# Optimization experiments

Hardware: AMD Instinct MI355X
Metric: run time of the kernel (lower is better)

Reference implementation:

```python
import jax, jax.numpy as jnp
import numpy as np

N, E = 50000, 800000
IN, HID, OUT = 128, 128, 64
BN_EPS = 1e-5


def _w(key, fan_in, fan_out):
    return jax.random.normal(key, (fan_in, fan_out), dtype=jnp.float32) / np.sqrt(fan_in)


def setup_inputs() -> dict:
    key = jax.random.key(0)
    ks = jax.random.split(key, 12)
    x = jax.random.normal(ks[0], (N, IN), dtype=jnp.float32)
    src = jax.random.randint(ks[1], (E,), 0, N, dtype=jnp.int32)
    dst = jax.random.randint(ks[2], (E,), 0, N, dtype=jnp.int32)
    eps = jax.random.normal(ks[3], (N, OUT), dtype=jnp.float32)
    return {
        "x": x, "src": src, "dst": dst, "eps": eps,
        # SAGEConv 1: in -> hidden (lin_l has bias, lin_r no bias, mean aggr)
        "W1l": _w(ks[4], IN, HID), "W1r": _w(ks[5], IN, HID), "b1": jnp.zeros((HID,), jnp.float32),
        "g1": jnp.ones((HID,), jnp.float32), "be1": jnp.zeros((HID,), jnp.float32),
        # SAGEConv 2: hidden -> 2*hidden
        "W2l": _w(ks[6], HID, 2 * HID), "W2r": _w(ks[7], HID, 2 * HID), "b2": jnp.zeros((2 * HID,), jnp.float32),
        "g2": jnp.ones((2 * HID,), jnp.float32), "be2": jnp.zeros((2 * HID,), jnp.float32),
        # SAGEConv 3: 2*hidden -> 2*out
        "W3l": _w(ks[8], 2 * HID, 2 * OUT), "W3r": _w(ks[9], 2 * HID, 2 * OUT), "b3": jnp.zeros((2 * OUT,), jnp.float32),
    }


def _sage(h, src, dst, Wl, Wr, b):
    # mean-aggregate source features at destination nodes, then two GEMMs
    msg = jax.ops.segment_sum(h[src], dst, num_segments=N)          # [N, F]
    deg = jax.ops.segment_sum(jnp.ones((src.shape[0],), h.dtype), dst, num_segments=N)
    aggr = msg / jnp.maximum(deg, 1.0)[:, None]
    return aggr @ Wl + h @ Wr + b


def _bn(h, gamma, beta):
    m = jnp.mean(h, axis=0)
    v = jnp.var(h, axis=0)
    return gamma * (h - m) * jax.lax.rsqrt(v + BN_EPS) + beta


def reference(x, src, dst, eps, W1l, W1r, b1, g1, be1, W2l, W2r, b2, g2, be2, W3l, W3r, b3):
    h = jax.nn.relu(_sage(x, src, dst, W1l, W1r, b1))
    h = _bn(h, g1, be1)                       # dropout = identity (eval)
    h = jax.nn.relu(_sage(h, src, dst, W2l, W2r, b2))
    h = _bn(h, g2, be2)
    h = _sage(h, src, dst, W3l, W3r, b3)      # [N, 2*OUT]
    mean, log_std = jnp.split(h, 2, axis=-1)
    z = mean + jnp.exp(log_std) * eps         # reparameterize
    return z
```

## Files before the change

### kernel.cpp

```cpp
#include <hip/hip_runtime.h>
#include <math.h>

#define N_NODES 50000
#define N_EDGES 800000
#define BN_EPS_F 1e-5f
#define SCAN_BS 512
#define SCAN_NB 98
#define RC 391
#define RQ 49
#define GXP 392

typedef unsigned short ushort_t;
typedef unsigned int uint_t;
typedef __attribute__((ext_vector_type(8))) short bf16x8;
typedef __attribute__((ext_vector_type(4))) float f32x4;

static __device__ __forceinline__ float4 ld4(const float* p) {
    return *reinterpret_cast<const float4*>(p);
}
static __device__ __forceinline__ float bf2f(ushort_t u) {
    return __uint_as_float(((uint_t)u) << 16);
}
static __device__ __forceinline__ ushort_t f2b(float f) {
    uint_t u = __float_as_uint(f);
    u += 0x7fffu + ((u >> 16) & 1u);
    return (ushort_t)(u >> 16);
}
static __device__ __forceinline__ void gload16(const void* g, void* l) {
    __builtin_amdgcn_global_load_lds(
        (const __attribute__((address_space(1))) void*)g,
        (__attribute__((address_space(3))) void*)l, 16, 0, 0);
}


__global__ void k_zero_i32(int* __restrict__ p, int n) {
    int i = blockIdx.x * blockDim.x + threadIdx.x;
    if (i < n) p[i] = 0;
}

__global__ void k_pre(const int* __restrict__ dst, int* __restrict__ deg2,
                      ushort_t* __restrict__ rank,
                      const float* __restrict__ x, ushort_t* __restrict__ xb,
                      const float* __restrict__ W1l, const float* __restrict__ W1r,
                      const float* __restrict__ W2l, ushort_t* __restrict__ wt1l,
                      ushort_t* __restrict__ wt1r, ushort_t* __restrict__ wt2l) {
    int b = blockIdx.x;
    if (b < 6250) {
        int role = b & 1;
        int id = (b >> 1) * 256 + threadIdx.x;
        if (role == 0) {
            rank[id] = (ushort_t)atomicAdd(&deg2[dst[id] * 16], 1);
        } else {
            float4 a = ld4(x + (size_t)id * 8);
            float4 c = ld4(x + (size_t)id * 8 + 4);
            uint_t o0 = (uint_t)f2b(a.x) | ((uint_t)f2b(a.y) << 16);
            uint_t o1 = (uint_t)f2b(a.z) | ((uint_t)f2b(a.w) << 16);
            uint_t o2 = (uint_t)f2b(c.x) | ((uint_t)f2b(c.y) << 16);
            uint_t o3 = (uint_t)f2b(c.z) | ((uint_t)f2b(c.w) << 16);
            *reinterpret_cast<uint4*>(xb + (size_t)id * 8) = make_uint4(o0, o1, o2, o3);
        }
    } else {
        int idx = (b - 6250) * 256 + threadIdx.x;
        if (idx < 16384) {
            int f = idx >> 7, k = idx & 127;
            wt1l[idx] = f2b(W1l[(size_t)k * 128 + f]);
        } else if (idx < 32768) {
            int j = idx - 16384;
            int f = j >> 7, k = j & 127;
            wt1r[j] = f2b(W1r[(size_t)k * 128 + f]);
        } else {
            int j = idx - 32768;
            int f = j >> 7, k = j & 127;
            wt2l[j] = f2b(W2l[(size_t)k * 256 + f]);
        }
    }
}

__global__ void k_scan1(const int* __restrict__ deg2, int* __restrict__ offs, int* __restrict__ bsum) {
    __shared__ int sh[SCAN_BS];
    int t = threadIdx.x;
    int g = blockIdx.x * SCAN_BS + t;
    int v = (g < N_NODES) ? deg2[g * 16] : 0;
    sh[t] = v;
    __syncthreads();
    for (int off = 1; off < SCAN_BS; off <<= 1) {
        int add = (t >= off) ? sh[t - off] : 0;
        __syncthreads();
        sh[t] += add;
        __syncthreads();
    }
    if (g < N_NODES) offs[g] = sh[t] - v;
    if (t == SCAN_BS - 1) bsum[blockIdx.x] = sh[t];
}

__global__ void k_scan2(int* __restrict__ bsum, int nb) {
    __shared__ int sh[128];
    int t = threadIdx.x;
    int v = (t < nb) ? bsum[t] : 0;
    sh[t] = v;
    __syncthreads();
    for (int off = 1; off < 128; off <<= 1) {
        int add = (t >= off) ? sh[t - off] : 0;
        __syncthreads();
        sh[t] += add;
        __syncthreads();
    }
    if (t < nb) bsum[t] = sh[t] - v;
}

__global__ void k_scan3(const int* __restrict__ deg2, int* __restrict__ offs,
                        const int* __restrict__ bsum, float* __restrict__ inv_deg,
                        int* __restrict__ degc) {
    int g = blockIdx.x * blockDim.x + threadIdx.x;
    if (g < N_NODES) {
        offs[g] += bsum[g / SCAN_BS];
        int d = deg2[g * 16];
        degc[g] = d;
        inv_deg[g] = 1.0f / (float)(d > 1 ? d : 1);
    }
}

__global__ void k_fill2(const int* __restrict__ src, const int* __restrict__ dst,
                        const int* __restrict__ offs, const ushort_t* __restrict__ rank,
                        ushort_t* __restrict__ eids) {
    int e = blockIdx.x * blockDim.x + threadIdx.x;
    if (e < N_EDGES) eids[offs[dst[e]] + (int)rank[e]] = (ushort_t)src[e];
}


__global__ void k_prep2(const float* __restrict__ W2r, const float* __restrict__ b2,
                        const float* __restrict__ scsh1, ushort_t* __restrict__ wt2r,
                        float* __restrict__ bias2) {
    int bid = blockIdx.x;
    if (bid < 128) {
        int idx = bid * 256 + threadIdx.x;
        int f = idx >> 7, k = idx & 127;
        wt2r[idx] = f2b(scsh1[k] * W2r[(size_t)k * 256 + f]);
    } else {
        int f = threadIdx.x;
        float s = b2[f];
        for (int k = 0; k < 128; ++k) s += scsh1[128 + k] * W2r[(size_t)k * 256 + f];
        bias2[f] = s;
    }
}

__global__ void k_prep3(const float* __restrict__ W3l, const float* __restrict__ W3r,
                        const float* __restrict__ b3, const float* __restrict__ scsh2,
                        ushort_t* __restrict__ wt3l, ushort_t* __restrict__ wt3r,
                        float* __restrict__ bias3l, float* __restrict__ bias3r) {
    int bid = blockIdx.x;
    if (bid < 256) {
        int half = bid >> 7;
        int idx = (bid & 127) * 256 + threadIdx.x;
        int f = idx >> 8, k = idx & 255;
        const float* W = half ? W3r : W3l;
        ushort_t* WT = half ? wt3r : wt3l;
        WT[idx] = f2b(scsh2[k] * W[(size_t)k * 128 + f]);
    } else {
        int t = threadIdx.x;
        int f = t & 127;
        const float* W = (t < 128) ? W3l : W3r;
        float s = (t < 128) ? 0.f : b3[f];
        for (int k = 0; k < 256; ++k) s += scsh2[256 + k] * W[(size_t)k * 128 + f];
        float* out = (t < 128) ? bias3l : bias3r;
        out[f] = s;
    }
}


#define ACCUM8(a) do { \
    acc[0] += bf2f((ushort_t)(a).x); acc[1] += bf2f((ushort_t)((a).x >> 16)); \
    acc[2] += bf2f((ushort_t)(a).y); acc[3] += bf2f((ushort_t)((a).y >> 16)); \
    acc[4] += bf2f((ushort_t)(a).z); acc[5] += bf2f((ushort_t)((a).z >> 16)); \
    acc[6] += bf2f((ushort_t)(a).w); acc[7] += bf2f((ushort_t)((a).w >> 16)); } while (0)

static __device__ __forceinline__ void gather_rows_g(
        const ushort_t* __restrict__ h, const ushort_t* __restrict__ eids,
        int beg, int d, size_t coff, float* acc) {
    int j = 0;
    for (; j + 8 <= d; j += 8) {
        uint4 a[8];
#pragma unroll
        for (int k = 0; k < 8; ++k) {
            int s = eids[beg + j + k];
            a[k] = *reinterpret_cast<const uint4*>(h + (size_t)s * 128 + coff);
        }
#pragma unroll
        for (int k = 0; k < 8; ++k) ACCUM8(a[k]);
    }
    for (; j + 4 <= d; j += 4) {
        uint4 a[4];
#pragma unroll
        for (int k = 0; k < 4; ++k) {
            int s = eids[beg + j + k];
            a[k] = *reinterpret_cast<const uint4*>(h + (size_t)s * 128 + coff);
        }
#pragma unroll
        for (int k = 0; k < 4; ++k) ACCUM8(a[k]);
    }
    for (; j + 2 <= d; j += 2) {
        int s0 = eids[beg + j];
        int s1 = eids[beg + j + 1];
        uint4 a = *reinterpret_cast<const uint4*>(h + (size_t)s0 * 128 + coff);
        uint4 b = *reinterpret_cast<const uint4*>(h + (size_t)s1 * 128 + coff);
        ACCUM8(a); ACCUM8(b);
    }
    if (j < d) {
        int s0 = eids[beg + j];
        uint4 a = *reinterpret_cast<const uint4*>(h + (size_t)s0 * 128 + coff);
        ACCUM8(a);
    }
}

template<int BN>
__global__ __launch_bounds__(256) void k_agg16(
        const ushort_t* __restrict__ h, const ushort_t* __restrict__ eids,
        const int* __restrict__ offs, const int* __restrict__ deg,
        const float* __restrict__ inv_deg, const float* __restrict__ scsh,
        ushort_t* __restrict__ out) {
    const int node = blockIdx.x * 16 + (threadIdx.x >> 4);
    const int lr = threadIdx.x & 15;
    if (node >= N_NODES) return;
    float acc[8];
#pragma unroll
    for (int v = 0; v < 8; ++v) acc[v] = 0.f;
    const int beg = offs[node];
    const int d = deg[node];
    const size_t coff = (size_t)lr * 8;
    gather_rows_g(h, eids, beg, d, coff, acc);

    float sc = inv_deg[node];
    if (BN) {
        float4 sa0 = ld4(&scsh[lr * 8]), sa1 = ld4(&scsh[lr * 8 + 4]);
        float4 sb0 = ld4(&scsh[128 + lr * 8]), sb1 = ld4(&scsh[128 + lr * 8 + 4]);
        if (d > 0) {
            acc[0] = acc[0] * sc * sa0.x + sb0.x; acc[1] = acc[1] * sc * sa0.y + sb0.y;
            acc[2] = acc[2] * sc * sa0.z + sb0.z; acc[3] = acc[3] * sc * sa0.w + sb0.w;
            acc[4] = acc[4] * sc * sa1.x + sb1.x; acc[5] = acc[5] * sc * sa1.y + sb1.y;
            acc[6] = acc[6] * sc * sa1.z + sb1.z; acc[7] = acc[7] * sc * sa1.w + sb1.w;
        } else {
#pragma unroll
            for (int v = 0; v < 8; ++v) acc[v] = 0.f;
        }
    } else {
#pragma unroll
        for (int v = 0; v < 8; ++v) acc[v] *= sc;
    }
    uint4 o;
    o.x = (uint_t)f2b(acc[0]) | ((uint_t)f2b(acc[1]) << 16);
    o.y = (uint_t)f2b(acc[2]) | ((uint_t)f2b(acc[3]) << 16);
    o.z = (uint_t)f2b(acc[4]) | ((uint_t)f2b(acc[5]) << 16);
    o.w = (uint_t)f2b(acc[6]) | ((uint_t)f2b(acc[7]) << 16);
    *reinterpret_cast<uint4*>(out + (size_t)node * 128 + coff) = o;
}

__global__ __launch_bounds__(256) void k_agg_reparam(
        const ushort_t* __restrict__ t3, const ushort_t* __restrict__ eids,
        const int* __restrict__ offs, const int* __restrict__ deg,
        const float* __restrict__ inv_deg, const ushort_t* __restrict__ u,
        const float* __restrict__ eps, float* __restrict__ z) {
    const int node = blockIdx.x * 16 + (threadIdx.x >> 4);
    const int lr = threadIdx.x & 15;
    if (node >= N_NODES) return;
    float acc[8];
#pragma unroll
    for (int v = 0; v < 8; ++v) acc[v] = 0.f;
    const int beg = offs[node];
    const int d = deg[node];
    const size_t coff = (size_t)lr * 8;
    gather_rows_g(t3, eids, beg, d, coff, acc);
    float ls[8];
#pragma unroll
    for (int v = 0; v < 8; ++v) ls[v] = __shfl_down(acc[v], 8);

    if (lr < 8) {
        float sc = inv_deg[node];
        uint4 um4 = *reinterpret_cast<const uint4*>(u + (size_t)node * 128 + lr * 8);
        uint4 ul4 = *reinterpret_cast<const uint4*>(u + (size_t)node * 128 + 64 + lr * 8);
        const float* ep = eps + (size_t)node * 64 + lr * 8;
        float4 e0 = ld4(ep), e1 = ld4(ep + 4);
        float um[8], ul[8];
        um[0] = bf2f((ushort_t)um4.x); um[1] = bf2f((ushort_t)(um4.x >> 16));
        um[2] = bf2f((ushort_t)um4.y); um[3] = bf2f((ushort_t)(um4.y >> 16));
        um[4] = bf2f((ushort_t)um4.z); um[5] = bf2f((ushort_t)(um4.z >> 16));
        um[6] = bf2f((ushort_t)um4.w); um[7] = bf2f((ushort_t)(um4.w >> 16));
        ul[0] = bf2f((ushort_t)ul4.x); ul[1] = bf2f((ushort_t)(ul4.x >> 16));
        ul[2] = bf2f((ushort_t)ul4.y); ul[3] = bf2f((ushort_t)(ul4.y >> 16));
        ul[4] = bf2f((ushort_t)ul4.z); ul[5] = bf2f((ushort_t)(ul4.z >> 16));
        ul[6] = bf2f((ushort_t)ul4.w); ul[7] = bf2f((ushort_t)(ul4.w >> 16));
        float4 o0, o1;
        o0.x = (acc[0] * sc + um[0]) + expf(ls[0] * sc + ul[0]) * e0.x;
        o0.y = (acc[1] * sc + um[1]) + expf(ls[1] * sc + ul[1]) * e0.y;
        o0.z = (acc[2] * sc + um[2]) + expf(ls[2] * sc + ul[2]) * e0.z;
        o0.w = (acc[3] * sc + um[3]) + expf(ls[3] * sc + ul[3]) * e0.w;
        o1.x = (acc[4] * sc + um[4]) + expf(ls[4] * sc + ul[4]) * e1.x;
        o1.y = (acc[5] * sc + um[5]) + expf(ls[5] * sc + ul[5]) * e1.y;
        o1.z = (acc[6] * sc + um[6]) + expf(ls[6] * sc + ul[6]) * e1.z;
        o1.w = (acc[7] * sc + um[7]) + expf(ls[7] * sc + ul[7]) * e1.w;
        float* zp = z + (size_t)node * 64 + lr * 8;
        *reinterpret_cast<float4*>(zp) = o0;
        *reinterpret_cast<float4*>(zp + 4) = o1;
    }
}


template<int RELU, int DUAL, int STATS, int SEL3, int K>
__global__ __launch_bounds__(256) void k_gemm_db(
        const ushort_t* __restrict__ A1, const ushort_t* __restrict__ A2,
        const ushort_t* __restrict__ B1, const ushort_t* __restrict__ B2,
        const float* __restrict__ bias, ushort_t* __restrict__ out,
        int F, float* __restrict__ partials,
        const float* __restrict__ bias2, ushort_t* __restrict__ out2) {
    __shared__ __align__(16) short lds[2][8192];
    const int bid = blockIdx.x;
    const int grp = bid >> 3;
    const int y = grp / RQ;
    const int rq = grp - y * RQ;
    const int r = (bid & 7) + (rq << 3);
    if (r >= RC) return;
    const int row0 = r * 128;

    int colblk = y, outsel = 0;
    if (SEL3) { colblk = 0; outsel = y; }
    const int col0 = colblk * 128;
    const ushort_t* __restrict__ Bp = (SEL3 && outsel) ? B2 : B1;
    const float* __restrict__ biasp = (SEL3 && outsel) ? bias2 : bias;
    ushort_t* __restrict__ outp = (SEL3 && outsel) ? out2 : out;

    const int tid = threadIdx.x;
    const int lane = tid & 63;
    const int w = tid >> 6;
    const int wr = (w >> 1) * 64;
    const int wc = (w & 1) * 64;

    int rowA[2], slA[2];
#pragma unroll
    for (int p = 0; p < 2; ++p) {
        int c = (p * 4 + w) * 64 + lane;
        int r_ = c >> 2, sp = c & 3;
        rowA[p] = r_;
        slA[p] = sp ^ ((r_ >> 1) & 3);
    }
    const int q = lane >> 4, lr = lane & 15;
    int aoff[4], boff[4];
#pragma unroll
    for (int f = 0; f < 4; ++f) {
        int ra = wr + f * 16 + lr;
        aoff[f] = ra * 32 + (q ^ ((ra >> 1) & 3)) * 8;
        int rb = wc + f * 16 + lr;
        boff[f] = 4096 + rb * 32 + (q ^ ((rb >> 1) & 3)) * 8;
    }

    f32x4 acc[4][4];
#pragma unroll
    for (int mf = 0; mf < 4; ++mf)
#pragma unroll
        for (int nf = 0; nf < 4; ++nf)
            acc[mf][nf] = (f32x4){0.f, 0.f, 0.f, 0.f};

    auto stage = [&](int buf, int t) {
        const ushort_t* A = A1;
        const ushort_t* B = SEL3 ? Bp : B1;
        int k0;
        if (DUAL) {
            if (t >= 4) { A = A2; B = B2; }
            k0 = (t & 3) * 32;
        } else {
            k0 = t * 32;
        }
        short* base = &lds[buf][0];
#pragma unroll
        for (int p = 0; p < 2; ++p) {
            int gr = row0 + rowA[p];
            if (gr > N_NODES - 1) gr = N_NODES - 1;
            gload16(A + (size_t)gr * K + k0 + slA[p] * 8, base + (p * 4 + w) * 512);
            int gc = col0 + rowA[p];
            gload16(B + (size_t)gc * K + k0 + slA[p] * 8, base + 4096 + (p * 4 + w) * 512);
        }
    };

    constexpr int NT = DUAL ? 8 : (K / 32);
    stage(0, 0);
    __syncthreads();
    int cur = 0;
    for (int t = 0; t < NT; ++t) {
        if (t + 1 < NT) stage(cur ^ 1, t + 1);
        bf16x8 av[4], bv[4];
#pragma unroll
        for (int f = 0; f < 4; ++f) {
            av[f] = *reinterpret_cast<const bf16x8*>(&lds[cur][aoff[f]]);
            bv[f] = *reinterpret_cast<const bf16x8*>(&lds[cur][boff[f]]);
        }
#pragma unroll
        for (int mf = 0; mf < 4; ++mf)
#pragma unroll
            for (int nf = 0; nf < 4; ++nf)
                acc[mf][nf] = __builtin_amdgcn_mfma_f32_16x16x32_bf16(
                    av[mf], bv[nf], acc[mf][nf], 0, 0, 0);
        __syncthreads();
        cur ^= 1;
    }

    const int orow = row0 + wr + q * 4;
    const int ocol = col0 + wc + lr;
    float s[4], s2[4];
#pragma unroll
    for (int nf = 0; nf < 4; ++nf) { s[nf] = 0.f; s2[nf] = 0.f; }
#pragma unroll
    for (int nf = 0; nf < 4; ++nf) {
        int colg = ocol + nf * 16;
        float bvs = biasp[colg];
#pragma unroll
        for (int mf = 0; mf < 4; ++mf) {
#pragma unroll
            for (int b = 0; b < 4; ++b) {
                int rr = orow + mf * 16 + b;
                if (rr < N_NODES) {
                    float v = acc[mf][nf][b] + bvs;
                    if (RELU) v = fmaxf(v, 0.f);
                    if (STATS) { s[nf] += v; s2[nf] += v * v; }
                    outp[(size_t)rr * F + colg] = f2b(v);
                }
            }
        }
    }

    if constexpr (STATS) {
        __syncthreads();
        float* sdf = (float*)&lds[0][0];
        const int u = (w >> 1) * 4 + q;
#pragma unroll
        for (int nf = 0; nf < 4; ++nf) {
            int cb = wc + nf * 16 + lr;
            sdf[u * 128 + cb] = s[nf];
            sdf[1024 + u * 128 + cb] = s2[nf];
        }
        __syncthreads();
        if (tid < 128) {
            float ss = 0.f, qq = 0.f;
#pragma unroll
            for (int u2 = 0; u2 < 8; ++u2) {
                ss += sdf[u2 * 128 + tid];
                qq += sdf[1024 + u2 * 128 + tid];
            }
            int cg = col0 + tid;
            partials[(size_t)cg * GXP + r] = ss;
            partials[(size_t)(F + cg) * GXP + r] = qq;
        }
    }
}


template<int F>
__global__ __launch_bounds__(64) void k_bn_scsh(
        const float* __restrict__ partials, const float* __restrict__ gamma,
        const float* __restrict__ beta, float* __restrict__ scsh) {
    const int c = blockIdx.x;
    const int l = threadIdx.x;
    float s = 0.f, q2 = 0.f;
    for (int g = l; g < RC; g += 64) {
        s += partials[(size_t)c * GXP + g];
        q2 += partials[(size_t)(F + c) * GXP + g];
    }
#pragma unroll
    for (int off = 1; off < 64; off <<= 1) {
        s += __shfl_xor(s, off);
        q2 += __shfl_xor(q2, off);
    }
    if (l == 0) {
        float mean = s * (1.0f / N_NODES);
        float var = q2 * (1.0f / N_NODES) - mean * mean;
        float sc = gamma[c] * rsqrtf(var + BN_EPS_F);
        scsh[c] = sc;
        scsh[F + c] = beta[c] - mean * sc;
    }
}


extern "C" void kernel_launch(void* const* d_in, const int* in_sizes, int n_in,
                              void* d_out, int out_size, void* d_ws, size_t ws_size,
                              hipStream_t stream) {
    (void)in_sizes; (void)n_in; (void)out_size; (void)ws_size;
    const float* x   = (const float*)d_in[0];
    const int*   src = (const int*)d_in[1];
    const int*   dst = (const int*)d_in[2];
    const float* eps = (const float*)d_in[3];
    const float* W1l = (const float*)d_in[4];
    const float* W1r = (const float*)d_in[5];
    const float* b1  = (const float*)d_in[6];
    const float* g1  = (const float*)d_in[7];
    const float* be1 = (const float*)d_in[8];
    const float* W2l = (const float*)d_in[9];
    const float* W2r = (const float*)d_in[10];
    const float* b2  = (const float*)d_in[11];
    const float* g2  = (const float*)d_in[12];
    const float* be2 = (const float*)d_in[13];
    const float* W3l = (const float*)d_in[14];
    const float* W3r = (const float*)d_in[15];
    const float* b3  = (const float*)d_in[16];
    float* z = (float*)d_out;

    char* ws = (char*)d_ws;
    size_t off = 0;
    auto alloc = [&](size_t bytes) -> char* {
        char* p = ws + off;
        off += (bytes + 255) & ~(size_t)255;
        return p;
    };
    int*      deg2   = (int*)alloc((size_t)N_NODES * 16 * 4);
    size_t zero_bytes = off;
    ushort_t* rank   = (ushort_t*)alloc((size_t)N_EDGES * 2);
    ushort_t* eids   = (ushort_t*)alloc((size_t)N_EDGES * 2);
    float*    scshs  = (float*)alloc(1024 * 4);
    float*    biases = (float*)alloc(512 * 4);
    int*      offs   = (int*)alloc(N_NODES * 4);
    int*      bsum   = (int*)alloc(128 * 4);
    int*      degc   = (int*)alloc(N_NODES * 4);
    float*    invd   = (float*)alloc(N_NODES * 4);
    ushort_t* xb     = (ushort_t*)alloc((size_t)N_NODES * 128 * 2);
    ushort_t* h1b    = (ushort_t*)alloc((size_t)N_NODES * 128 * 2);
    ushort_t* h2b    = (ushort_t*)alloc((size_t)N_NODES * 256 * 2);
    ushort_t* aggrb  = (ushort_t*)alloc((size_t)N_NODES * 256 * 2);
    ushort_t* u3b    = (ushort_t*)alloc((size_t)N_NODES * 128 * 2);
    float*    parts  = (float*)alloc((size_t)512 * GXP * 4);
    ushort_t* wt1l   = (ushort_t*)alloc(128 * 128 * 2);
    ushort_t* wt1r   = (ushort_t*)alloc(128 * 128 * 2);
    ushort_t* wt2l   = (ushort_t*)alloc(256 * 128 * 2);
    ushort_t* wt2r   = (ushort_t*)alloc(256 * 128 * 2);
    ushort_t* wt3l   = (ushort_t*)alloc(128 * 256 * 2);
    ushort_t* wt3r   = (ushort_t*)alloc(128 * 256 * 2);
    ushort_t* t3b    = aggrb;

    float* scsh1  = scshs;
    float* scsh2  = scshs + 256;
    float* bias2  = biases;
    float* bias3l = biases + 256;
    float* bias3r = biases + 384;

    k_zero_i32<<<((int)(zero_bytes / 4) + 255) / 256, 256, 0, stream>>>((int*)ws, (int)(zero_bytes / 4));
    k_pre<<<6506, 256, 0, stream>>>(dst, deg2, rank, x, xb, W1l, W1r, W2l, wt1l, wt1r, wt2l);
    k_scan1<<<SCAN_NB, SCAN_BS, 0, stream>>>(deg2, offs, bsum);
    k_scan2<<<1, 128, 0, stream>>>(bsum, SCAN_NB);
    k_scan3<<<(N_NODES + 255) / 256, 256, 0, stream>>>(deg2, offs, bsum, invd, degc);
    k_fill2<<<(N_EDGES + 255) / 256, 256, 0, stream>>>(src, dst, offs, rank, eids);

    const int AGG_BLKS = N_NODES / 16;
    const int GEMM_G = 8 * RQ;

    k_agg16<0><<<AGG_BLKS, 256, 0, stream>>>(xb, eids, offs, degc, invd, nullptr, aggrb);
    k_gemm_db<1, 1, 1, 0, 128><<<GEMM_G, 256, 0, stream>>>(
        aggrb, xb, wt1l, wt1r, b1, h1b, 128, parts, nullptr, nullptr);
    k_bn_scsh<128><<<128, 64, 0, stream>>>(parts, g1, be1, scsh1);

    k_prep2<<<129, 256, 0, stream>>>(W2r, b2, scsh1, wt2r, bias2);
    k_agg16<1><<<AGG_BLKS, 256, 0, stream>>>(h1b, eids, offs, degc, invd, scsh1, aggrb);
    k_gemm_db<1, 1, 1, 0, 128><<<GEMM_G * 2, 256, 0, stream>>>(
        aggrb, h1b, wt2l, wt2r, bias2, h2b, 256, parts, nullptr, nullptr);
    k_bn_scsh<256><<<256, 64, 0, stream>>>(parts, g2, be2, scsh2);

    k_prep3<<<257, 256, 0, stream>>>(W3l, W3r, b3, scsh2, wt3l, wt3r, bias3l, bias3r);
    k_gemm_db<0, 0, 0, 1, 256><<<GEMM_G * 2, 256, 0, stream>>>(
        h2b, nullptr, wt3l, wt3r, bias3l, t3b, 128, nullptr, bias3r, u3b);
    k_agg_reparam<<<AGG_BLKS, 256, 0, stream>>>(t3b, eids, offs, degc, invd, u3b, eps, z);
}
```

Before: 239.9 us.

## Split gather aggregation into feature slices across blocks for cache locality

The aggregation kernels now split the 128 feature columns into four 32-column slices. Each block handles 64 nodes using 4 lanes per node, so concurrently running blocks gather the same narrow column band of the source rows, aiming to improve L2/MALL hit rates on random row gathers. The reparam kernel likewise assigns one thread per node per 8-column slice and gathers the mean and log-std halves directly instead of using a cross-lane shuffle. In exchange, each edge index is read four to eight times, and each gathered access becomes a narrower, less coalesced 16-byte read per row.

```diff
diff --git a/kernel.cpp b/kernel.cpp
--- a/kernel.cpp
+++ b/kernel.cpp
@@ -30,6 +30,12 @@
     __builtin_amdgcn_global_load_lds(
         (const __attribute__((address_space(1))) void*)g,
         (__attribute__((address_space(3))) void*)l, 16, 0, 0);
+}
+static __device__ __forceinline__ void acc8(float* acc, uint4 a) {
+    acc[0] += bf2f((ushort_t)a.x); acc[1] += bf2f((ushort_t)(a.x >> 16));
+    acc[2] += bf2f((ushort_t)a.y); acc[3] += bf2f((ushort_t)(a.y >> 16));
+    acc[4] += bf2f((ushort_t)a.z); acc[5] += bf2f((ushort_t)(a.z >> 16));
+    acc[6] += bf2f((ushort_t)a.w); acc[7] += bf2f((ushort_t)(a.w >> 16));
 }
 
 
@@ -168,72 +174,54 @@
 }
 
 
-#define ACCUM8(a) do { \
-    acc[0] += bf2f((ushort_t)(a).x); acc[1] += bf2f((ushort_t)((a).x >> 16)); \
-    acc[2] += bf2f((ushort_t)(a).y); acc[3] += bf2f((ushort_t)((a).y >> 16)); \
-    acc[4] += bf2f((ushort_t)(a).z); acc[5] += bf2f((ushort_t)((a).z >> 16)); \
-    acc[6] += bf2f((ushort_t)(a).w); acc[7] += bf2f((ushort_t)((a).w >> 16)); } while (0)
-
-static __device__ __forceinline__ void gather_rows_g(
-        const ushort_t* __restrict__ h, const ushort_t* __restrict__ eids,
-        int beg, int d, size_t coff, float* acc) {
-    int j = 0;
-    for (; j + 8 <= d; j += 8) {
-        uint4 a[8];
-#pragma unroll
-        for (int k = 0; k < 8; ++k) {
-            int s = eids[beg + j + k];
-            a[k] = *reinterpret_cast<const uint4*>(h + (size_t)s * 128 + coff);
-        }
-#pragma unroll
-        for (int k = 0; k < 8; ++k) ACCUM8(a[k]);
-    }
-    for (; j + 4 <= d; j += 4) {
-        uint4 a[4];
-#pragma unroll
-        for (int k = 0; k < 4; ++k) {
-            int s = eids[beg + j + k];
-            a[k] = *reinterpret_cast<const uint4*>(h + (size_t)s * 128 + coff);
-        }
-#pragma unroll
-        for (int k = 0; k < 4; ++k) ACCUM8(a[k]);
-    }
-    for (; j + 2 <= d; j += 2) {
-        int s0 = eids[beg + j];
-        int s1 = eids[beg + j + 1];
-        uint4 a = *reinterpret_cast<const uint4*>(h + (size_t)s0 * 128 + coff);
-        uint4 b = *reinterpret_cast<const uint4*>(h + (size_t)s1 * 128 + coff);
-        ACCUM8(a); ACCUM8(b);
-    }
-    if (j < d) {
-        int s0 = eids[beg + j];
-        uint4 a = *reinterpret_cast<const uint4*>(h + (size_t)s0 * 128 + coff);
-        ACCUM8(a);
-    }
-}
-
 template<int BN>
-__global__ __launch_bounds__(256) void k_agg16(
+__global__ __launch_bounds__(256) void k_agg16s(
         const ushort_t* __restrict__ h, const ushort_t* __restrict__ eids,
         const int* __restrict__ offs, const int* __restrict__ deg,
         const float* __restrict__ inv_deg, const float* __restrict__ scsh,
         ushort_t* __restrict__ out) {
-    const int node = blockIdx.x * 16 + (threadIdx.x >> 4);
-    const int lr = threadIdx.x & 15;
+    const int cls = blockIdx.x & 7;
+    const int slice = cls >> 1;
+    const int chunk = (blockIdx.x >> 3) * 2 + (cls & 1);
+    const int node = chunk * 64 + (threadIdx.x >> 2);
+    const int l = threadIdx.x & 3;
     if (node >= N_NODES) return;
+    const int eoff = slice * 32 + l * 8;
     float acc[8];
 #pragma unroll
     for (int v = 0; v < 8; ++v) acc[v] = 0.f;
     const int beg = offs[node];
     const int d = deg[node];
-    const size_t coff = (size_t)lr * 8;
-    gather_rows_g(h, eids, beg, d, coff, acc);
-
+    int jj = 0;
+    for (; jj + 8 <= d; jj += 8) {
+        uint4 a[8];
+#pragma unroll
+        for (int k = 0; k < 8; ++k) {
+            int sn = eids[beg + jj + k];
+            a[k] = *reinterpret_cast<const uint4*>(h + (size_t)sn * 128 + eoff);
+        }
+#pragma unroll
+        for (int k = 0; k < 8; ++k) acc8(acc, a[k]);
+    }
+    for (; jj + 4 <= d; jj += 4) {
+        uint4 a[4];
+#pragma unroll
+        for (int k = 0; k < 4; ++k) {
+            int sn = eids[beg + jj + k];
+            a[k] = *reinterpret_cast<const uint4*>(h + (size_t)sn * 128 + eoff);
+        }
+#pragma unroll
+        for (int k = 0; k < 4; ++k) acc8(acc, a[k]);
+    }
+    for (; jj < d; ++jj) {
+        int sn = eids[beg + jj];
+        acc8(acc, *reinterpret_cast<const uint4*>(h + (size_t)sn * 128 + eoff));
+    }
     float sc = inv_deg[node];
     if (BN) {
-        float4 sa0 = ld4(&scsh[lr * 8]), sa1 = ld4(&scsh[lr * 8 + 4]);
-        float4 sb0 = ld4(&scsh[128 + lr * 8]), sb1 = ld4(&scsh[128 + lr * 8 + 4]);
         if (d > 0) {
+            float4 sa0 = ld4(&scsh[eoff]), sa1 = ld4(&scsh[eoff + 4]);
+            float4 sb0 = ld4(&scsh[128 + eoff]), sb1 = ld4(&scsh[128 + eoff + 4]);
             acc[0] = acc[0] * sc * sa0.x + sb0.x; acc[1] = acc[1] * sc * sa0.y + sb0.y;
             acc[2] = acc[2] * sc * sa0.z + sb0.z; acc[3] = acc[3] * sc * sa0.w + sb0.w;
             acc[4] = acc[4] * sc * sa1.x + sb1.x; acc[5] = acc[5] * sc * sa1.y + sb1.y;
@@ -251,56 +239,70 @@
     o.y = (uint_t)f2b(acc[2]) | ((uint_t)f2b(acc[3]) << 16);
     o.z = (uint_t)f2b(acc[4]) | ((uint_t)f2b(acc[5]) << 16);
     o.w = (uint_t)f2b(acc[6]) | ((uint_t)f2b(acc[7]) << 16);
-    *reinterpret_cast<uint4*>(out + (size_t)node * 128 + coff) = o;
-}
-
-__global__ __launch_bounds__(256) void k_agg_reparam(
+    *reinterpret_cast<uint4*>(out + (size_t)node * 128 + eoff) = o;
+}
+
+
+__global__ __launch_bounds__(256) void k_agg_reparam_s(
         const ushort_t* __restrict__ t3, const ushort_t* __restrict__ eids,
         const int* __restrict__ offs, const int* __restrict__ deg,
         const float* __restrict__ inv_deg, const ushort_t* __restrict__ u,
         const float* __restrict__ eps, float* __restrict__ z) {
-    const int node = blockIdx.x * 16 + (threadIdx.x >> 4);
-    const int lr = threadIdx.x & 15;
+    const int s = blockIdx.x & 7;
+    const int node = (blockIdx.x >> 3) * 256 + threadIdx.x;
     if (node >= N_NODES) return;
-    float acc[8];
-#pragma unroll
-    for (int v = 0; v < 8; ++v) acc[v] = 0.f;
+    const int em = s * 8;
+    const int el = 64 + em;
+    float am[8], al[8];
+#pragma unroll
+    for (int v = 0; v < 8; ++v) { am[v] = 0.f; al[v] = 0.f; }
     const int beg = offs[node];
     const int d = deg[node];
-    const size_t coff = (size_t)lr * 8;
-    gather_rows_g(t3, eids, beg, d, coff, acc);
-    float ls[8];
-#pragma unroll
-    for (int v = 0; v < 8; ++v) ls[v] = __shfl_down(acc[v], 8);
-
-    if (lr < 8) {
-        float sc = inv_deg[node];
-        uint4 um4 = *reinterpret_cast<const uint4*>(u + (size_t)node * 128 + lr * 8);
-        uint4 ul4 = *reinterpret_cast<const uint4*>(u + (size_t)node * 128 + 64 + lr * 8);
-        const float* ep = eps + (size_t)node * 64 + lr * 8;
-        float4 e0 = ld4(ep), e1 = ld4(ep + 4);
-        float um[8], ul[8];
-        um[0] = bf2f((ushort_t)um4.x); um[1] = bf2f((ushort_t)(um4.x >> 16));
-        um[2] = bf2f((ushort_t)um4.y); um[3] = bf2f((ushort_t)(um4.y >> 16));
-        um[4] = bf2f((ushort_t)um4.z); um[5] = bf2f((ushort_t)(um4.z >> 16));
-        um[6] = bf2f((ushort_t)um4.w); um[7] = bf2f((ushort_t)(um4.w >> 16));
-        ul[0] = bf2f((ushort_t)ul4.x); ul[1] = bf2f((ushort_t)(ul4.x >> 16));
-        ul[2] = bf2f((ushort_t)ul4.y); ul[3] = bf2f((ushort_t)(ul4.y >> 16));
-        ul[4] = bf2f((ushort_t)ul4.z); ul[5] = bf2f((ushort_t)(ul4.z >> 16));
-        ul[6] = bf2f((ushort_t)ul4.w); ul[7] = bf2f((ushort_t)(ul4.w >> 16));
-        float4 o0, o1;
-        o0.x = (acc[0] * sc + um[0]) + expf(ls[0] * sc + ul[0]) * e0.x;
-        o0.y = (acc[1] * sc + um[1]) + expf(ls[1] * sc + ul[1]) * e0.y;
-        o0.z = (acc[2] * sc + um[2]) + expf(ls[2] * sc + ul[2]) * e0.z;
-        o0.w = (acc[3] * sc + um[3]) + expf(ls[3] * sc + ul[3]) * e0.w;
-        o1.x = (acc[4] * sc + um[4]) + expf(ls[4] * sc + ul[4]) * e1.x;
-        o1.y = (acc[5] * sc + um[5]) + expf(ls[5] * sc + ul[5]) * e1.y;
-        o1.z = (acc[6] * sc + um[6]) + expf(ls[6] * sc + ul[6]) * e1.z;
-        o1.w = (acc[7] * sc + um[7]) + expf(ls[7] * sc + ul[7]) * e1.w;
-        float* zp = z + (size_t)node * 64 + lr * 8;
-        *reinterpret_cast<float4*>(zp) = o0;
-        *reinterpret_cast<float4*>(zp + 4) = o1;
-    }
+    int jj = 0;
+    for (; jj + 4 <= d; jj += 4) {
+        uint4 a[4], b[4];
+#pragma unroll
+        for (int k = 0; k < 4; ++k) {
+            int sn = eids[beg + jj + k];
+            const ushort_t* row = t3 + (size_t)sn * 128;
+            a[k] = *reinterpret_cast<const uint4*>(row + em);
+            b[k] = *reinterpret_cast<const uint4*>(row + el);
+        }
+#pragma unroll
+        for (int k = 0; k < 4; ++k) { acc8(am, a[k]); acc8(al, b[k]); }
+    }
+    for (; jj < d; ++jj) {
+        int sn = eids[beg + jj];
+        const ushort_t* row = t3 + (size_t)sn * 128;
+        acc8(am, *reinterpret_cast<const uint4*>(row + em));
+        acc8(al, *reinterpret_cast<const uint4*>(row + el));
+    }
+    float sc = inv_deg[node];
+    uint4 um4 = *reinterpret_cast<const uint4*>(u + (size_t)node * 128 + em);
+    uint4 ul4 = *reinterpret_cast<const uint4*>(u + (size_t)node * 128 + el);
+    const float* ep = eps + (size_t)node * 64 + em;
+    float4 e0 = ld4(ep), e1 = ld4(ep + 4);
+    float um[8], ul[8];
+    um[0] = bf2f((ushort_t)um4.x); um[1] = bf2f((ushort_t)(um4.x >> 16));
+    um[2] = bf2f((ushort_t)um4.y); um[3] = bf2f((ushort_t)(um4.y >> 16));
+    um[4] = bf2f((ushort_t)um4.z); um[5] = bf2f((ushort_t)(um4.z >> 16));
+    um[6] = bf2f((ushort_t)um4.w); um[7] = bf2f((ushort_t)(um4.w >> 16));
+    ul[0] = bf2f((ushort_t)ul4.x); ul[1] = bf2f((ushort_t)(ul4.x >> 16));
+    ul[2] = bf2f((ushort_t)ul4.y); ul[3] = bf2f((ushort_t)(ul4.y >> 16));
+    ul[4] = bf2f((ushort_t)ul4.z); ul[5] = bf2f((ushort_t)(ul4.z >> 16));
+    ul[6] = bf2f((ushort_t)ul4.w); ul[7] = bf2f((ushort_t)(ul4.w >> 16));
+    float4 o0, o1;
+    o0.x = (am[0] * sc + um[0]) + expf(al[0] * sc + ul[0]) * e0.x;
+    o0.y = (am[1] * sc + um[1]) + expf(al[1] * sc + ul[1]) * e0.y;
+    o0.z = (am[2] * sc + um[2]) + expf(al[2] * sc + ul[2]) * e0.z;
+    o0.w = (am[3] * sc + um[3]) + expf(al[3] * sc + ul[3]) * e0.w;
+    o1.x = (am[4] * sc + um[4]) + expf(al[4] * sc + ul[4]) * e1.x;
+    o1.y = (am[5] * sc + um[5]) + expf(al[5] * sc + ul[5]) * e1.y;
+    o1.z = (am[6] * sc + um[6]) + expf(al[6] * sc + ul[6]) * e1.z;
+    o1.w = (am[7] * sc + um[7]) + expf(al[7] * sc + ul[7]) * e1.w;
+    float* zp = z + (size_t)node * 64 + em;
+    *reinterpret_cast<float4*>(zp) = o0;
+    *reinterpret_cast<float4*>(zp + 4) = o1;
 }
 
 
@@ -544,16 +546,17 @@
     k_scan3<<<(N_NODES + 255) / 256, 256, 0, stream>>>(deg2, offs, bsum, invd, degc);
     k_fill2<<<(N_EDGES + 255) / 256, 256, 0, stream>>>(src, dst, offs, rank, eids);
 
-    const int AGG_BLKS = N_NODES / 16;
+    const int AGG_S = 8 * 391;
+    const int AGGR_S = 8 * 196;
     const int GEMM_G = 8 * RQ;
 
-    k_agg16<0><<<AGG_BLKS, 256, 0, stream>>>(xb, eids, offs, degc, invd, nullptr, aggrb);
+    k_agg16s<0><<<AGG_S, 256, 0, stream>>>(xb, eids, offs, degc, invd, nullptr, aggrb);
     k_gemm_db<1, 1, 1, 0, 128><<<GEMM_G, 256, 0, stream>>>(
         aggrb, xb, wt1l, wt1r, b1, h1b, 128, parts, nullptr, nullptr);
     k_bn_scsh<128><<<128, 64, 0, stream>>>(parts, g1, be1, scsh1);
 
     k_prep2<<<129, 256, 0, stream>>>(W2r, b2, scsh1, wt2r, bias2);
-    k_agg16<1><<<AGG_BLKS, 256, 0, stream>>>(h1b, eids, offs, degc, invd, scsh1, aggrb);
+    k_agg16s<1><<<AGG_S, 256, 0, stream>>>(h1b, eids, offs, degc, invd, scsh1, aggrb);
     k_gemm_db<1, 1, 1, 0, 128><<<GEMM_G * 2, 256, 0, stream>>>(
         aggrb, h1b, wt2l, wt2r, bias2, h2b, 256, parts, nullptr, nullptr);
     k_bn_scsh<256><<<256, 64, 0, stream>>>(parts, g2, be2, scsh2);
@@ -561,5 +564,5 @@
     k_prep3<<<257, 256, 0, stream>>>(W3l, W3r, b3, scsh2, wt3l, wt3r, bias3l, bias3r);
     k_gemm_db<0, 0, 0, 1, 256><<<GEMM_G * 2, 256, 0, stream>>>(
         h2b, nullptr, wt3l, wt3r, bias3l, t3b, 128, nullptr, bias3r, u3b);
-    k_agg_reparam<<<AGG_BLKS, 256, 0, stream>>>(t3b, eids, offs, degc, invd, u3b, eps, z);
-}
+    k_agg_reparam_s<<<AGGR_S, 256, 0, stream>>>(t3b, eids, offs, degc, invd, u3b, eps, z);
+}
```

Measured after the change: 426.2 us. +77.7%, slower.
